# Performance work log

Hardware: AMD Instinct MI355X
Metric: run time of the kernel (lower is better)

The kernel has to match this reference:

```python
import jax, jax.numpy as jnp
import numpy as np

N_NODES = 50000
N_EDGES = 800000
DIM_IN = 128
DIM_OUT = 64
HEADS = 4
NEG_SLOPE = 0.2


def setup_inputs() -> dict:
    key = jax.random.key(0)
    k_x, k_e, k_w, k_a = jax.random.split(key, 4)
    x = jax.random.normal(k_x, (N_NODES, DIM_IN), dtype=jnp.float32)
    edge_index = jax.random.randint(k_e, (2, N_EDGES), 0, N_NODES, dtype=jnp.int32)
    # Stacked per-head params: W (Linear(dim_in, dim_out, bias=False)) and
    # a (Linear(2*dim_out, 1, bias=False)) for each of HEADS heads.
    W = jax.random.normal(k_w, (HEADS, DIM_IN, DIM_OUT), dtype=jnp.float32) * (1.0 / np.sqrt(DIM_IN))
    a = jax.random.normal(k_a, (HEADS, 2 * DIM_OUT), dtype=jnp.float32) * (1.0 / np.sqrt(2 * DIM_OUT))
    return {"x": x, "edge_index": edge_index, "W": W, "a": a}


def _gat_forward(x, W, a, edge_index):
    src = edge_index[0]  # segment for softmax / scatter target
    dst = edge_index[1]  # node whose features are gathered (x_j)
    # h: [N, H, D]
    h = jnp.einsum('nd,hdo->nho', x, W)
    a_i = a[:, :DIM_OUT]   # [H, D] applied to x_i
    a_j = a[:, DIM_OUT:]   # [H, D] applied to x_j
    # per-node attention logit halves: [N, H]
    s_i = jnp.einsum('nhd,hd->nh', h, a_i)
    s_j = jnp.einsum('nhd,hd->nh', h, a_j)
    e = jax.nn.leaky_relu(s_i[src] + s_j[dst], NEG_SLOPE)  # [E, H]
    # segment softmax over edges grouped by src node
    m = jax.ops.segment_max(e, src, num_segments=N_NODES)  # [N, H]
    ex = jnp.exp(e - m[src])
    denom = jax.ops.segment_sum(ex, src, num_segments=N_NODES)  # [N, H]
    att = ex / denom[src]  # [E, H]
    # weighted scatter-sum of gathered features: [N, H, D]
    msgs = att[:, :, None] * h[dst]
    h_prime = jax.ops.segment_sum(msgs, src, num_segments=N_NODES)
    # concat=False -> mean over heads
    return jnp.mean(h_prime, axis=1)  # [N, D]


def reference(x, edge_index, W, a):
    return _gat_forward(x, W, a, edge_index)
```

## Files before the change

### kernel.cpp

```cpp
#include <hip/hip_runtime.h>
#include <hip/hip_bf16.h>

#define N_NODES 50000
#define N_EDGES 800000
#define DIM_IN  128
#define DIM_OUT 64
#define HEADS   4
#define NEG_SLOPE 0.2f
#define NPB 32
#define GEMM_BLOCKS ((N_NODES + NPB - 1) / NPB)
#define N_PAD (GEMM_BLOCKS * NPB)
#define PAD 64
#define EPT 16
#define SCAT_THREADS (N_EDGES / EPT)
#define SCAT_BLOCKS ((SCAT_THREADS + 255) / 256)
#define FAT_GRID (GEMM_BLOCKS + SCAT_BLOCKS)
#define XROW 136
#define LTROW 260
#define CSTRIDE 16
#define PREP_BLOCKS 64

typedef __attribute__((ext_vector_type(8))) short short8;
typedef __attribute__((ext_vector_type(4))) short short4v;
typedef __attribute__((ext_vector_type(4))) float f32x4;

__device__ __forceinline__ unsigned int f2bf(float f) {
    unsigned int u = __float_as_uint(f);
    return (u + 0x7FFFu + ((u >> 16) & 1u)) >> 16;
}
__device__ __forceinline__ float bf2f(unsigned int b) {
    return __uint_as_float(b << 16);
}

__global__ __launch_bounds__(256) void prep_kernel(
    const float* __restrict__ W, unsigned short* __restrict__ Wph,
    unsigned short* __restrict__ Wpl, int* __restrict__ cursor)
{
    const int b = blockIdx.x;
    const int t = threadIdx.x;
    if (b < 16) {
        const int i = b * 256 + t;
        const int lane = i & 63, nt = (i >> 6) & 3, kc = (i >> 8) & 3, h = (i >> 10) & 3;
        const int col = lane & 15, quad = lane >> 4;
        unsigned short hv[8], lv[8];
#pragma unroll
        for (int j = 0; j < 8; ++j) {
            const int k = kc * 32 + quad * 8 + j;
            const int n = nt * 16 + col;
            const float f = W[h * (DIM_IN * DIM_OUT) + k * DIM_OUT + n];
            const unsigned int hb = f2bf(f);
            hv[j] = (unsigned short)hb;
            lv[j] = (unsigned short)f2bf(f - bf2f(hb));
        }
        *(short8*)(Wph + (size_t)i * 8) = *(short8*)hv;
        *(short8*)(Wpl + (size_t)i * 8) = *(short8*)lv;
    } else {
        int4* c4 = (int4*)cursor;
        const int total = N_NODES * CSTRIDE / 4;
        for (int i = (b - 16) * 256 + t; i < total; i += (PREP_BLOCKS - 16) * 256)
            c4[i] = make_int4(0, 0, 0, 0);
    }
}

__global__ __launch_bounds__(256) void fat_kernel(
    const float* __restrict__ x, const unsigned short* __restrict__ Wph,
    const unsigned short* __restrict__ Wpl, const float* __restrict__ a,
    unsigned short* __restrict__ h2, float* __restrict__ s_i, float* __restrict__ s_j,
    const int* __restrict__ ei, int* __restrict__ cursor, unsigned short* __restrict__ sdst)
{
    __shared__ __align__(16) unsigned char smem[2 * NPB * XROW * 2];
    const int b = blockIdx.x;
    const int t = threadIdx.x;

    if (b >= GEMM_BLOCKS) {
        const int i = (b - GEMM_BLOCKS) * 256 + t;
        if (i < SCAT_THREADS) {
            const int e0 = i * EPT;
            int srcs[EPT], dsts[EPT], rr[EPT];
#pragma unroll
            for (int q = 0; q < 4; ++q) {
                *(int4*)(srcs + 4 * q) = *(const int4*)(ei + e0 + 4 * q);
                *(int4*)(dsts + 4 * q) = *(const int4*)(ei + N_EDGES + e0 + 4 * q);
            }
#pragma unroll
            for (int q = 0; q < EPT; ++q)
                rr[q] = atomicAdd(&cursor[srcs[q] * CSTRIDE], 1);
#pragma unroll
            for (int q = 0; q < EPT; ++q)
                if (rr[q] < PAD) sdst[srcs[q] * PAD + rr[q]] = (unsigned short)dsts[q];
        }
        return;
    }

    short* xh = (short*)smem;
    short* xl = xh + NPB * XROW;
    const int nb = b * NPB;

    {
        const float4* xg = (const float4*)x;
        const int base = nb * (DIM_IN / 4);
        const int limit = N_NODES * (DIM_IN / 4);
#pragma unroll
        for (int r = 0; r < 4; ++r) {
            const int idx = t + 256 * r;
            const int gi = base + idx;
            float4 v = {0.f, 0.f, 0.f, 0.f};
            if (gi < limit) v = xg[gi];
            const int node = idx >> 5;
            const int dg = (idx & 31) * 4;
            unsigned short hs[4], ls[4];
            const float fv[4] = {v.x, v.y, v.z, v.w};
#pragma unroll
            for (int c = 0; c < 4; ++c) {
                const unsigned int hb = f2bf(fv[c]);
                hs[c] = (unsigned short)hb;
                ls[c] = (unsigned short)f2bf(fv[c] - bf2f(hb));
            }
            *(short4v*)(xh + node * XROW + dg) = *(short4v*)hs;
            *(short4v*)(xl + node * XROW + dg) = *(short4v*)ls;
        }
    }
    __syncthreads();

    const int w = t >> 6;
    const int lane = t & 63;
    const int col = lane & 15, quad = lane >> 4;

    f32x4 acc[2][4];
#pragma unroll
    for (int mt = 0; mt < 2; ++mt)
#pragma unroll
        for (int nt = 0; nt < 4; ++nt) acc[mt][nt] = (f32x4){0.f, 0.f, 0.f, 0.f};

    const short8* Bh = (const short8*)Wph;
    const short8* Bl = (const short8*)Wpl;
#pragma unroll
    for (int kc = 0; kc < 4; ++kc) {
        const short8 ah0 = *(const short8*)(xh + (0 * 16 + col) * XROW + kc * 32 + quad * 8);
        const short8 al0 = *(const short8*)(xl + (0 * 16 + col) * XROW + kc * 32 + quad * 8);
        const short8 ah1 = *(const short8*)(xh + (1 * 16 + col) * XROW + kc * 32 + quad * 8);
        const short8 al1 = *(const short8*)(xl + (1 * 16 + col) * XROW + kc * 32 + quad * 8);
#pragma unroll
        for (int nt = 0; nt < 4; ++nt) {
            const int fi = ((w * 4 + kc) * 4 + nt) * 64 + lane;
            const short8 bh = Bh[fi];
            const short8 bl = Bl[fi];
            acc[0][nt] = __builtin_amdgcn_mfma_f32_16x16x32_bf16(ah0, bh, acc[0][nt], 0, 0, 0);
            acc[0][nt] = __builtin_amdgcn_mfma_f32_16x16x32_bf16(al0, bh, acc[0][nt], 0, 0, 0);
            acc[0][nt] = __builtin_amdgcn_mfma_f32_16x16x32_bf16(ah0, bl, acc[0][nt], 0, 0, 0);
            acc[1][nt] = __builtin_amdgcn_mfma_f32_16x16x32_bf16(ah1, bh, acc[1][nt], 0, 0, 0);
            acc[1][nt] = __builtin_amdgcn_mfma_f32_16x16x32_bf16(al1, bh, acc[1][nt], 0, 0, 0);
            acc[1][nt] = __builtin_amdgcn_mfma_f32_16x16x32_bf16(ah1, bl, acc[1][nt], 0, 0, 0);
        }
    }

    float aiv[4], ajv[4];
#pragma unroll
    for (int nt = 0; nt < 4; ++nt) {
        aiv[nt] = a[w * (2 * DIM_OUT) + nt * 16 + col];
        ajv[nt] = a[w * (2 * DIM_OUT) + DIM_OUT + nt * 16 + col];
    }
#pragma unroll
    for (int mt = 0; mt < 2; ++mt) {
#pragma unroll
        for (int r = 0; r < 4; ++r) {
            float pi = 0.f, pj = 0.f;
#pragma unroll
            for (int nt = 0; nt < 4; ++nt) {
                pi = fmaf(acc[mt][nt][r], aiv[nt], pi);
                pj = fmaf(acc[mt][nt][r], ajv[nt], pj);
            }
#pragma unroll
            for (int off = 8; off > 0; off >>= 1) {
                pi += __shfl_down(pi, off, 16);
                pj += __shfl_down(pj, off, 16);
            }
            if (col == 0) {
                const int n = nb + mt * 16 + quad * 4 + r;
                s_i[n * HEADS + w] = pi;
                s_j[n * HEADS + w] = pj;
            }
        }
    }
    __syncthreads();

    short* lt = (short*)smem;
#pragma unroll
    for (int mt = 0; mt < 2; ++mt)
#pragma unroll
        for (int nt = 0; nt < 4; ++nt)
#pragma unroll
            for (int r = 0; r < 4; ++r)
                lt[(mt * 16 + quad * 4 + r) * LTROW + (nt * 16 + col) * 4 + w] =
                    (short)f2bf(acc[mt][nt][r]);
    __syncthreads();

    uint2* hg = (uint2*)(h2 + (size_t)nb * (DIM_OUT * HEADS));
#pragma unroll
    for (int r = 0; r < 8; ++r) {
        const int idx = t + 256 * r;
        const int node = idx >> 6;
        const int wo = idx & 63;
        hg[idx] = *(const uint2*)(lt + node * LTROW + wo * 4);
    }
}

__global__ __launch_bounds__(256) void fused_kernel(
    const int* __restrict__ cursor, const unsigned short* __restrict__ sdst,
    const float* __restrict__ s_i, const float* __restrict__ s_j,
    const unsigned short* __restrict__ h2, float* __restrict__ out)
{
    __shared__ float4 att_s[4][64];
    __shared__ int    dst_s[4][64];
    const int wid = (blockIdx.x * 256 + threadIdx.x) >> 6;
    const int w = (threadIdx.x >> 6) & 3;
    const int lane = threadIdx.x & 63;
    if (wid >= N_NODES) return;
    const int n = wid;
    const int d = min(cursor[n * CSTRIDE], PAD);
    const int start = n * PAD;

    float acc = 0.f;
    if (d > 0) {
        const float4 si = *(const float4*)(s_i + n * HEADS);
        float4 m4 = {-INFINITY, -INFINITY, -INFINITY, -INFINITY};
        float4 cz = {-INFINITY, -INFINITY, -INFINITY, -INFINITY};
        int cdst = 0;
        if (lane < d) {
            cdst = (int)sdst[start + lane];
            const float4 sj = *(const float4*)(s_j + cdst * HEADS);
            float z0 = si.x + sj.x, z1 = si.y + sj.y, z2 = si.z + sj.z, z3 = si.w + sj.w;
            cz.x = z0 >= 0.f ? z0 : NEG_SLOPE * z0;
            cz.y = z1 >= 0.f ? z1 : NEG_SLOPE * z1;
            cz.z = z2 >= 0.f ? z2 : NEG_SLOPE * z2;
            cz.w = z3 >= 0.f ? z3 : NEG_SLOPE * z3;
            m4 = cz;
        }
#pragma unroll
        for (int off = 32; off > 0; off >>= 1) {
            m4.x = fmaxf(m4.x, __shfl_xor(m4.x, off, 64));
            m4.y = fmaxf(m4.y, __shfl_xor(m4.y, off, 64));
            m4.z = fmaxf(m4.z, __shfl_xor(m4.z, off, 64));
            m4.w = fmaxf(m4.w, __shfl_xor(m4.w, off, 64));
        }
        float4 ex = {0.f, 0.f, 0.f, 0.f};
        if (lane < d) {
            ex.x = __expf(cz.x - m4.x);
            ex.y = __expf(cz.y - m4.y);
            ex.z = __expf(cz.z - m4.z);
            ex.w = __expf(cz.w - m4.w);
        }
        float4 sm = ex;
#pragma unroll
        for (int off = 32; off > 0; off >>= 1) {
            sm.x += __shfl_xor(sm.x, off, 64);
            sm.y += __shfl_xor(sm.y, off, 64);
            sm.z += __shfl_xor(sm.z, off, 64);
            sm.w += __shfl_xor(sm.w, off, 64);
        }
        if (lane < d) {
            att_s[w][lane] = make_float4(ex.x / sm.x, ex.y / sm.y, ex.z / sm.z, ex.w / sm.w);
            dst_s[w][lane] = cdst;
        }

        const unsigned short* hbase = h2 + lane * HEADS;
        int e = 0;
        for (; e + 8 <= d; e += 8) {
            uint2 hv[8];
            float4 at[8];
#pragma unroll
            for (int q = 0; q < 8; ++q) {
                const int dd = dst_s[w][e + q];
                at[q] = att_s[w][e + q];
                hv[q] = *(const uint2*)(hbase + (size_t)dd * (DIM_OUT * HEADS));
            }
#pragma unroll
            for (int q = 0; q < 8; ++q) {
                acc += at[q].x * bf2f(hv[q].x & 0xFFFFu) + at[q].y * bf2f(hv[q].x >> 16)
                     + at[q].z * bf2f(hv[q].y & 0xFFFFu) + at[q].w * bf2f(hv[q].y >> 16);
            }
        }
        for (; e + 4 <= d; e += 4) {
            uint2 hv[4];
            float4 at[4];
#pragma unroll
            for (int q = 0; q < 4; ++q) {
                const int dd = dst_s[w][e + q];
                at[q] = att_s[w][e + q];
                hv[q] = *(const uint2*)(hbase + (size_t)dd * (DIM_OUT * HEADS));
            }
#pragma unroll
            for (int q = 0; q < 4; ++q) {
                acc += at[q].x * bf2f(hv[q].x & 0xFFFFu) + at[q].y * bf2f(hv[q].x >> 16)
                     + at[q].z * bf2f(hv[q].y & 0xFFFFu) + at[q].w * bf2f(hv[q].y >> 16);
            }
        }
        for (; e < d; ++e) {
            const int dd = dst_s[w][e];
            const float4 a4 = att_s[w][e];
            const uint2 hv = *(const uint2*)(hbase + (size_t)dd * (DIM_OUT * HEADS));
            acc += a4.x * bf2f(hv.x & 0xFFFFu) + a4.y * bf2f(hv.x >> 16)
                 + a4.z * bf2f(hv.y & 0xFFFFu) + a4.w * bf2f(hv.y >> 16);
        }
    }
    out[n * DIM_OUT + lane] = 0.25f * acc;
}

extern "C" void kernel_launch(void* const* d_in, const int* in_sizes, int n_in,
                              void* d_out, int out_size, void* d_ws, size_t ws_size,
                              hipStream_t stream) {
    const float* x  = (const float*)d_in[0];
    const int*   ei = (const int*)d_in[1];
    const float* W  = (const float*)d_in[2];
    const float* a  = (const float*)d_in[3];
    float* out = (float*)d_out;

    char* ws = (char*)d_ws;
    size_t off = 0;
    auto alloc = [&](size_t bytes) { void* p = ws + off; off = (off + bytes + 511) & ~size_t(511); return p; };
    unsigned short* h2  = (unsigned short*)alloc(sizeof(unsigned short) * N_PAD * DIM_OUT * HEADS);
    float* s_i    = (float*)alloc(sizeof(float) * N_PAD * HEADS);
    float* s_j    = (float*)alloc(sizeof(float) * N_PAD * HEADS);
    int*   cursor = (int*)alloc(sizeof(int) * N_NODES * CSTRIDE);
    unsigned short* sdst = (unsigned short*)alloc(sizeof(unsigned short) * N_NODES * PAD);
    unsigned short* Wph  = (unsigned short*)alloc(sizeof(unsigned short) * HEADS * DIM_IN * DIM_OUT);
    unsigned short* Wpl  = (unsigned short*)alloc(sizeof(unsigned short) * HEADS * DIM_IN * DIM_OUT);

    prep_kernel<<<PREP_BLOCKS, 256, 0, stream>>>(W, Wph, Wpl, cursor);

    fat_kernel<<<FAT_GRID, 256, 0, stream>>>(x, Wph, Wpl, a, h2, s_i, s_j, ei, cursor, sdst);

    const int fb = (N_NODES * 64 + 255) / 256;
    fused_kernel<<<fb, 256, 0, stream>>>(cursor, sdst, s_i, s_j, h2, out);
}
```

Before: 190.5 us.

## Replace global-atomic edge bucketing with chunked LDS histogram, scan, and scatter

Global atomics on a padded per-node cursor are replaced by a three-phase counting sort. Each of 128 edge chunks builds a packed 16-bit per-node histogram in shared memory. A column-wise exclusive scan across chunks runs inside the GEMM kernel's extra blocks. A separate scatter kernel then places destinations using LDS atomics seeded with the scanned offsets. This removes contended global atomics and the zero-init pass, at the cost of an extra kernel launch, a roughly 12 MB count buffer read and written several times, and only 128 blocks for the count and scatter phases.

```diff
diff --git a/kernel.cpp b/kernel.cpp
--- a/kernel.cpp
+++ b/kernel.cpp
@@ -11,14 +11,14 @@
 #define GEMM_BLOCKS ((N_NODES + NPB - 1) / NPB)
 #define N_PAD (GEMM_BLOCKS * NPB)
 #define PAD 64
-#define EPT 16
-#define SCAT_THREADS (N_EDGES / EPT)
-#define SCAT_BLOCKS ((SCAT_THREADS + 255) / 256)
-#define FAT_GRID (GEMM_BLOCKS + SCAT_BLOCKS)
+#define CHUNKS 128
+#define EPC (N_EDGES / CHUNKS)
+#define CPITCH 50048
+#define HWORDS (CPITCH / 2)
+#define SCAN_BLOCKS ((HWORDS + 255) / 256)
+#define FAT_GRID (SCAN_BLOCKS + GEMM_BLOCKS)
 #define XROW 136
 #define LTROW 260
-#define CSTRIDE 16
-#define PREP_BLOCKS 64
 
 typedef __attribute__((ext_vector_type(8))) short short8;
 typedef __attribute__((ext_vector_type(4))) short short4v;
@@ -32,14 +32,16 @@
     return __uint_as_float(b << 16);
 }
 
-__global__ __launch_bounds__(256) void prep_kernel(
+__global__ __launch_bounds__(512) void prep_count_kernel(
     const float* __restrict__ W, unsigned short* __restrict__ Wph,
-    unsigned short* __restrict__ Wpl, int* __restrict__ cursor)
+    unsigned short* __restrict__ Wpl, const int* __restrict__ ei,
+    unsigned short* __restrict__ cnt)
 {
+    __shared__ unsigned int hist[HWORDS];
     const int b = blockIdx.x;
     const int t = threadIdx.x;
-    if (b < 16) {
-        const int i = b * 256 + t;
+    if (b < 8) {
+        const int i = b * 512 + t;
         const int lane = i & 63, nt = (i >> 6) & 3, kc = (i >> 8) & 3, h = (i >> 10) & 3;
         const int col = lane & 15, quad = lane >> 4;
         unsigned short hv[8], lv[8];
@@ -54,47 +56,58 @@
         }
         *(short8*)(Wph + (size_t)i * 8) = *(short8*)hv;
         *(short8*)(Wpl + (size_t)i * 8) = *(short8*)lv;
-    } else {
-        int4* c4 = (int4*)cursor;
-        const int total = N_NODES * CSTRIDE / 4;
-        for (int i = (b - 16) * 256 + t; i < total; i += (PREP_BLOCKS - 16) * 256)
-            c4[i] = make_int4(0, 0, 0, 0);
-    }
+        return;
+    }
+    const int c = b - 8;
+    for (int i = t; i < HWORDS; i += 512) hist[i] = 0;
+    __syncthreads();
+    const int* srcp = ei + c * EPC;
+    for (int e = t; e < EPC; e += 512) {
+        const int s = srcp[e];
+        atomicAdd(&hist[s >> 1], 1u << ((s & 1) * 16));
+    }
+    __syncthreads();
+    unsigned int* rowp = (unsigned int*)(cnt + (size_t)c * CPITCH);
+    for (int i = t; i < HWORDS; i += 512) rowp[i] = hist[i];
 }
 
 __global__ __launch_bounds__(256) void fat_kernel(
     const float* __restrict__ x, const unsigned short* __restrict__ Wph,
     const unsigned short* __restrict__ Wpl, const float* __restrict__ a,
     unsigned short* __restrict__ h2, float* __restrict__ s_i, float* __restrict__ s_j,
-    const int* __restrict__ ei, int* __restrict__ cursor, unsigned short* __restrict__ sdst)
+    unsigned short* __restrict__ cnt, int* __restrict__ cursor)
 {
     __shared__ __align__(16) unsigned char smem[2 * NPB * XROW * 2];
     const int b = blockIdx.x;
     const int t = threadIdx.x;
 
-    if (b >= GEMM_BLOCKS) {
-        const int i = (b - GEMM_BLOCKS) * 256 + t;
-        if (i < SCAT_THREADS) {
-            const int e0 = i * EPT;
-            int srcs[EPT], dsts[EPT], rr[EPT];
-#pragma unroll
-            for (int q = 0; q < 4; ++q) {
-                *(int4*)(srcs + 4 * q) = *(const int4*)(ei + e0 + 4 * q);
-                *(int4*)(dsts + 4 * q) = *(const int4*)(ei + N_EDGES + e0 + 4 * q);
-            }
-#pragma unroll
-            for (int q = 0; q < EPT; ++q)
-                rr[q] = atomicAdd(&cursor[srcs[q] * CSTRIDE], 1);
-#pragma unroll
-            for (int q = 0; q < EPT; ++q)
-                if (rr[q] < PAD) sdst[srcs[q] * PAD + rr[q]] = (unsigned short)dsts[q];
+    if (b < SCAN_BLOCKS) {
+        const int i = b * 256 + t;
+        if (i < HWORDS) {
+            unsigned int* p = (unsigned int*)cnt + i;
+            unsigned int runlo = 0, runhi = 0;
+#pragma unroll
+            for (int c0 = 0; c0 < CHUNKS; c0 += 16) {
+                unsigned int v[16];
+#pragma unroll
+                for (int q = 0; q < 16; ++q) v[q] = p[(size_t)(c0 + q) * HWORDS];
+#pragma unroll
+                for (int q = 0; q < 16; ++q) {
+                    p[(size_t)(c0 + q) * HWORDS] = runlo | (runhi << 16);
+                    runlo += v[q] & 0xFFFFu;
+                    runhi += v[q] >> 16;
+                }
+            }
+            const int n0 = i * 2;
+            if (n0 < N_NODES) cursor[n0] = (int)runlo;
+            if (n0 + 1 < N_NODES) cursor[n0 + 1] = (int)runhi;
         }
         return;
     }
 
     short* xh = (short*)smem;
     short* xl = xh + NPB * XROW;
-    const int nb = b * NPB;
+    const int nb = (b - SCAN_BLOCKS) * NPB;
 
     {
         const float4* xg = (const float4*)x;
@@ -202,6 +215,28 @@
         const int node = idx >> 6;
         const int wo = idx & 63;
         hg[idx] = *(const uint2*)(lt + node * LTROW + wo * 4);
+    }
+}
+
+__global__ __launch_bounds__(512) void scatter_kernel(
+    const int* __restrict__ ei, const unsigned short* __restrict__ cnt,
+    unsigned short* __restrict__ sdst)
+{
+    __shared__ unsigned int cur[HWORDS];
+    const int c = blockIdx.x;
+    const int t = threadIdx.x;
+    const unsigned int* rowp = (const unsigned int*)(cnt + (size_t)c * CPITCH);
+    for (int i = t; i < HWORDS; i += 512) cur[i] = rowp[i];
+    __syncthreads();
+    const int* srcp = ei + c * EPC;
+    const int* dstp = ei + N_EDGES + c * EPC;
+    for (int e = t; e < EPC; e += 512) {
+        const int s = srcp[e];
+        const int d = dstp[e];
+        const unsigned int sh = (unsigned int)(s & 1) * 16u;
+        const unsigned int old = atomicAdd(&cur[s >> 1], 1u << sh);
+        const unsigned int slot = (old >> sh) & 0xFFFFu;
+        if (slot < PAD) sdst[s * PAD + slot] = (unsigned short)d;
     }
 }
 
@@ -217,7 +252,7 @@
     const int lane = threadIdx.x & 63;
     if (wid >= N_NODES) return;
     const int n = wid;
-    const int d = min(cursor[n * CSTRIDE], PAD);
+    const int d = min(cursor[n], PAD);
     const int start = n * PAD;
 
     float acc = 0.f;
@@ -321,14 +356,17 @@
     unsigned short* h2  = (unsigned short*)alloc(sizeof(unsigned short) * N_PAD * DIM_OUT * HEADS);
     float* s_i    = (float*)alloc(sizeof(float) * N_PAD * HEADS);
     float* s_j    = (float*)alloc(sizeof(float) * N_PAD * HEADS);
-    int*   cursor = (int*)alloc(sizeof(int) * N_NODES * CSTRIDE);
+    int*   cursor = (int*)alloc(sizeof(int) * N_NODES);
     unsigned short* sdst = (unsigned short*)alloc(sizeof(unsigned short) * N_NODES * PAD);
+    unsigned short* cnt  = (unsigned short*)alloc(sizeof(unsigned short) * CHUNKS * CPITCH);
     unsigned short* Wph  = (unsigned short*)alloc(sizeof(unsigned short) * HEADS * DIM_IN * DIM_OUT);
     unsigned short* Wpl  = (unsigned short*)alloc(sizeof(unsigned short) * HEADS * DIM_IN * DIM_OUT);
 
-    prep_kernel<<<PREP_BLOCKS, 256, 0, stream>>>(W, Wph, Wpl, cursor);
-
-    fat_kernel<<<FAT_GRID, 256, 0, stream>>>(x, Wph, Wpl, a, h2, s_i, s_j, ei, cursor, sdst);
+    prep_count_kernel<<<8 + CHUNKS, 512, 0, stream>>>(W, Wph, Wpl, ei, cnt);
+
+    fat_kernel<<<FAT_GRID, 256, 0, stream>>>(x, Wph, Wpl, a, h2, s_i, s_j, cnt, cursor);
+
+    scatter_kernel<<<CHUNKS, 512, 0, stream>>>(ei, cnt, sdst);
 
     const int fb = (N_NODES * 64 + 255) / 256;
     fused_kernel<<<fb, 256, 0, stream>>>(cursor, sdst, s_i, s_j, h2, out);
```

After: 180.1 us. -5.4%, faster.
